# Kernel optimization log

Hardware: AMD Instinct MI355X
Metric: run time of the kernel (lower is better)

Reference implementation:

```python
import jax, jax.numpy as jnp
import numpy as np

N_NODES = 100000
D_FEAT = 256
INPUT_ATT = 256


def setup_inputs() -> dict:
    key = jax.random.key(0)
    k1, k2, k3, kw, kh = jax.random.split(key, 5)
    x1 = jax.random.normal(k1, (N_NODES, D_FEAT), dtype=jnp.float32)
    x2 = jax.random.normal(k2, (N_NODES, D_FEAT), dtype=jnp.float32)
    x3 = jax.random.normal(k3, (N_NODES, D_FEAT), dtype=jnp.float32)
    # xavier-normal-like init for parameters
    W = jax.random.normal(kw, (INPUT_ATT, N_NODES), dtype=jnp.float32) * float(np.sqrt(2.0 / (INPUT_ATT + N_NODES)))
    h_n = jax.random.normal(kh, (1, INPUT_ATT), dtype=jnp.float32) * float(np.sqrt(2.0 / (1 + INPUT_ATT)))
    return {"x1": x1, "x2": x2, "x3": x3, "W": W, "h_n": h_n}


def reference(x1, x2, x3, W, h_n):
    # temp_k = tanh(W @ x_k): (input_att, D) for each of the 3 views
    t1 = jnp.tanh(W @ x1)
    t2 = jnp.tanh(W @ x2)
    t3 = jnp.tanh(W @ x3)
    # per-view, per-feature score: (1, D) each -> stacked (3, D)
    scores = jnp.concatenate([h_n @ t1, h_n @ t2, h_n @ t3], axis=0)  # (3, D)
    beta = jax.nn.softmax(scores, axis=0)  # softmax over the 3 views, per feature column
    # fused broadcast weighted sum (replaces the per-row Python loop)
    out = beta[0] * x1 + beta[1] * x2 + beta[2] * x3  # (N, D)
    return out
```

## Files before the change

### kernel.cpp

```cpp
#include <hip/hip_runtime.h>
#include <hip/hip_bf16.h>

#define N_NODES 100000
#define D_FEAT  256
#define N_ATT   256

typedef __bf16 bf16x4 __attribute__((ext_vector_type(4)));
typedef __bf16 bf16x8 __attribute__((ext_vector_type(8)));
typedef float  f32x16 __attribute__((ext_vector_type(16)));

__device__ __forceinline__ unsigned short bf16_rne(float f) {
    unsigned u = __float_as_uint(f);
    return (unsigned short)((u + 0x7fffu + ((u >> 16) & 1u)) >> 16);
}

__device__ __forceinline__ void split1(float f, unsigned short& h, unsigned short& l) {
    h = bf16_rne(f);
    float fh = __uint_as_float((unsigned)h << 16);
    l = (unsigned short)(__float_as_uint(f - fh) >> 16);
}

__device__ __forceinline__ bf16x8 ld8(const unsigned short* p) {
    bf16x4 lo = *(const bf16x4*)p;
    bf16x4 hi = *(const bf16x4*)(p + 4);
    return __builtin_shufflevector(lo, hi, 0, 1, 2, 3, 4, 5, 6, 7);
}

#define LDK 36

__global__ __launch_bounds__(512, 4) void gemm_split(
    const float* __restrict__ x1, const float* __restrict__ x2,
    const float* __restrict__ x3, const float* __restrict__ W,
    float* __restrict__ C, int chunk)
{
    extern __shared__ unsigned short lds[];
    unsigned short* Ah = lds;
    unsigned short* Al = Ah + 128 * LDK;
    unsigned short* Bh = Al + 128 * LDK;

    const int bid = blockIdx.x;
    const int s   = bid / 6;
    const int pos = bid % 6;
    const int v   = pos >> 1;
    const int m0  = (pos & 1) * 128;
    const float* __restrict__ X = (v == 0) ? x1 : (v == 1) ? x2 : x3;

    const int ks = s * chunk;
    const int ke = min(ks + chunk, N_NODES);

    const int tid  = threadIdx.x;
    const int lane = tid & 63;
    const int wave = tid >> 6;
    const int mstrip = (wave & 3) * 32;
    const int nhalf  = (wave >> 2) * 128;

    const int a_m  = tid >> 3;
    const int a_kk = (tid & 7) * 4;
    const int b_n64 = tid & 63;
    const int b_nb  = (tid >> 8) * 64;
    const int b_kq  = ((tid >> 6) & 3) ^ ((tid >> 3) & 3);

    const int l31 = lane & 31;
    const int khalf = (lane >> 5) * 8;

    f32x16 acc[4] = {};

    float4 pa[2];
    float  pb[4][4];

    auto issue = [&](int kg0) {
        #pragma unroll
        for (int p = 0; p < 2; ++p) {
            int kg = kg0 + a_kk;
            pa[p] = make_float4(0.f, 0.f, 0.f, 0.f);
            if (kg < ke)
                pa[p] = *(const float4*)(W + (size_t)(m0 + p * 64 + a_m) * N_NODES + kg);
        }
        #pragma unroll
        for (int p = 0; p < 4; ++p) {
            int n  = (p >> 1) * 128 + b_nb + b_n64;
            int kg = kg0 + (p & 1) * 16 + b_kq * 4;
            pb[p][0] = pb[p][1] = pb[p][2] = pb[p][3] = 0.f;
            if (kg < ke) {
                const float* xp = X + (size_t)kg * D_FEAT + n;
                pb[p][0] = xp[0];
                pb[p][1] = xp[D_FEAT];
                pb[p][2] = xp[2 * D_FEAT];
                pb[p][3] = xp[3 * D_FEAT];
            }
        }
    };

    issue(ks);

    for (int k0 = ks; k0 < ke; k0 += 32) {
        __syncthreads();

        #pragma unroll
        for (int p = 0; p < 2; ++p) {
            ushort4 h4, l4;
            split1(pa[p].x, h4.x, l4.x); split1(pa[p].y, h4.y, l4.y);
            split1(pa[p].z, h4.z, l4.z); split1(pa[p].w, h4.w, l4.w);
            int m = p * 64 + a_m;
            *(ushort4*)(Ah + m * LDK + a_kk) = h4;
            *(ushort4*)(Al + m * LDK + a_kk) = l4;
        }
        #pragma unroll
        for (int p = 0; p < 4; ++p) {
            int n  = (p >> 1) * 128 + b_nb + b_n64;
            int kb = (p & 1) * 16 + b_kq * 4;
            ushort4 h4;
            h4.x = bf16_rne(pb[p][0]); h4.y = bf16_rne(pb[p][1]);
            h4.z = bf16_rne(pb[p][2]); h4.w = bf16_rne(pb[p][3]);
            *(ushort4*)(Bh + n * LDK + kb) = h4;
        }

        if (k0 + 32 < ke) issue(k0 + 32);

        __syncthreads();

        #pragma unroll
        for (int kk = 0; kk < 2; ++kk) {
            int kf = kk * 16 + khalf;
            int arow = mstrip + l31;
            bf16x8 ah = ld8(Ah + arow * LDK + kf);
            bf16x8 al = ld8(Al + arow * LDK + kf);
            #pragma unroll
            for (int nb = 0; nb < 4; ++nb) {
                int brow = nhalf + nb * 32 + l31;
                bf16x8 bh = ld8(Bh + brow * LDK + kf);
                acc[nb] = __builtin_amdgcn_mfma_f32_32x32x16_bf16(ah, bh, acc[nb], 0, 0, 0);
                acc[nb] = __builtin_amdgcn_mfma_f32_32x32x16_bf16(al, bh, acc[nb], 0, 0, 0);
            }
        }
    }

    float* Cv = C + v * (N_ATT * D_FEAT);
    const int col = l31;
    const int rbase = 4 * (lane >> 5);
    #pragma unroll
    for (int nb = 0; nb < 4; ++nb) {
        int gj = nhalf + nb * 32 + col;
        #pragma unroll
        for (int r = 0; r < 16; ++r) {
            int row = (r & 3) + 8 * (r >> 2) + rbase;
            int gi = m0 + mstrip + row;
            unsafeAtomicAdd(Cv + gi * D_FEAT + gj, acc[nb][r]);
        }
    }
}

__global__ __launch_bounds__(256) void score_kernel(
    const float* __restrict__ C, const float* __restrict__ h,
    float* __restrict__ scores)
{
    const int v  = blockIdx.x >> 3;
    const int ig = blockIdx.x & 7;
    const int j  = threadIdx.x;
    const float* Cv = C + v * (N_ATT * D_FEAT);
    float s = 0.f;
    #pragma unroll 4
    for (int i = ig * 32; i < ig * 32 + 32; ++i)
        s += h[i] * tanhf(Cv[i * D_FEAT + j]);
    unsafeAtomicAdd(scores + v * D_FEAT + j, s);
}

__device__ __forceinline__ float blend(float xa, float xb, float xc,
                                       float t0, float t1, float t2) {
    float m = fmaxf(t0, fmaxf(t1, t2));
    float e0 = __expf(t0 - m), e1 = __expf(t1 - m), e2 = __expf(t2 - m);
    float inv = 1.0f / (e0 + e1 + e2);
    return (e0 * xa + e1 * xb + e2 * xc) * inv;
}

__global__ __launch_bounds__(256) void out_kernel(
    const float* __restrict__ x1, const float* __restrict__ x2,
    const float* __restrict__ x3, const float* __restrict__ scores,
    float* __restrict__ out)
{
    size_t idx  = (size_t)blockIdx.x * 256 + threadIdx.x;
    size_t base = idx * 4;
    int j = (int)(base & (D_FEAT - 1));
    float4 a = *(const float4*)(x1 + base);
    float4 b = *(const float4*)(x2 + base);
    float4 c = *(const float4*)(x3 + base);
    float4 s0 = *(const float4*)(scores + j);
    float4 s1 = *(const float4*)(scores + D_FEAT + j);
    float4 s2 = *(const float4*)(scores + 2 * D_FEAT + j);
    float4 o;
    o.x = blend(a.x, b.x, c.x, s0.x, s1.x, s2.x);
    o.y = blend(a.y, b.y, c.y, s0.y, s1.y, s2.y);
    o.z = blend(a.z, b.z, c.z, s0.z, s1.z, s2.z);
    o.w = blend(a.w, b.w, c.w, s0.w, s1.w, s2.w);
    *(float4*)(out + base) = o;
}

extern "C" void kernel_launch(void* const* d_in, const int* in_sizes, int n_in,
                              void* d_out, int out_size, void* d_ws, size_t ws_size,
                              hipStream_t stream) {
    const float* x1 = (const float*)d_in[0];
    const float* x2 = (const float*)d_in[1];
    const float* x3 = (const float*)d_in[2];
    const float* W  = (const float*)d_in[3];
    const float* h  = (const float*)d_in[4];
    float* out = (float*)d_out;

    float* C      = (float*)d_ws;
    float* scores = C + 3 * N_ATT * D_FEAT;

    hipMemsetAsync(d_ws, 0, (3 * N_ATT * D_FEAT + 3 * D_FEAT) * sizeof(float), stream);

    const int chunk = 1180;
    gemm_split<<<dim3(510), dim3(512), 512 * LDK * 2, stream>>>(x1, x2, x3, W, C, chunk);

    score_kernel<<<dim3(24), dim3(256), 0, stream>>>(C, h, scores);

    out_kernel<<<dim3((N_NODES * D_FEAT) / (4 * 256)), dim3(256), 0, stream>>>(
        x1, x2, x3, scores, out);
}
```

Before: 505.5 us.

## Double-buffer LDS tiles in split-K GEMM with one barrier per step

Splits the GEMM k-loop into stage and compute steps over two LDS buffers. Each iteration now issues the next global loads, runs MFMAs on the current buffer, then converts and stores into the other buffer, so it needs one barrier per step instead of two. The chunk size becomes a multiple of 32, which lets the per-element bounds checks on W and X loads be dropped. The cost is double the LDS per block, which may lower how many blocks fit on a CU, and the code now relies on N being divisible by the tile size.

```diff
diff --git a/kernel.cpp b/kernel.cpp
--- a/kernel.cpp
+++ b/kernel.cpp
@@ -27,6 +27,7 @@
 }
 
 #define LDK 36
+#define BUF_SHORTS (512 * LDK)
 
 __global__ __launch_bounds__(512, 4) void gemm_split(
     const float* __restrict__ x1, const float* __restrict__ x2,
@@ -34,9 +35,6 @@
     float* __restrict__ C, int chunk)
 {
     extern __shared__ unsigned short lds[];
-    unsigned short* Ah = lds;
-    unsigned short* Al = Ah + 128 * LDK;
-    unsigned short* Bh = Al + 128 * LDK;
 
     const int bid = blockIdx.x;
     const int s   = bid / 6;
@@ -54,48 +52,41 @@
     const int mstrip = (wave & 3) * 32;
     const int nhalf  = (wave >> 2) * 128;
 
-    const int a_m  = tid >> 3;
-    const int a_kk = (tid & 7) * 4;
+    const int a_m   = tid >> 3;
+    const int a_kk  = (tid & 7) * 4;
     const int b_n64 = tid & 63;
     const int b_nb  = (tid >> 8) * 64;
-    const int b_kq  = ((tid >> 6) & 3) ^ ((tid >> 3) & 3);
+    const int b_kq4 = (((tid >> 6) & 3) ^ ((tid >> 3) & 3)) * 4;
 
     const int l31 = lane & 31;
     const int khalf = (lane >> 5) * 8;
 
     f32x16 acc[4] = {};
-
     float4 pa[2];
     float  pb[4][4];
 
+    const float* Wb = W + (size_t)(m0 + a_m) * N_NODES + a_kk;
+
     auto issue = [&](int kg0) {
         #pragma unroll
-        for (int p = 0; p < 2; ++p) {
-            int kg = kg0 + a_kk;
-            pa[p] = make_float4(0.f, 0.f, 0.f, 0.f);
-            if (kg < ke)
-                pa[p] = *(const float4*)(W + (size_t)(m0 + p * 64 + a_m) * N_NODES + kg);
-        }
+        for (int p = 0; p < 2; ++p)
+            pa[p] = *(const float4*)(Wb + (size_t)p * 64 * N_NODES + kg0);
         #pragma unroll
         for (int p = 0; p < 4; ++p) {
             int n  = (p >> 1) * 128 + b_nb + b_n64;
-            int kg = kg0 + (p & 1) * 16 + b_kq * 4;
-            pb[p][0] = pb[p][1] = pb[p][2] = pb[p][3] = 0.f;
-            if (kg < ke) {
-                const float* xp = X + (size_t)kg * D_FEAT + n;
-                pb[p][0] = xp[0];
-                pb[p][1] = xp[D_FEAT];
-                pb[p][2] = xp[2 * D_FEAT];
-                pb[p][3] = xp[3 * D_FEAT];
-            }
+            int kg = kg0 + (p & 1) * 16 + b_kq4;
+            const float* xp = X + (size_t)kg * D_FEAT + n;
+            pb[p][0] = xp[0];
+            pb[p][1] = xp[D_FEAT];
+            pb[p][2] = xp[2 * D_FEAT];
+            pb[p][3] = xp[3 * D_FEAT];
         }
     };
 
-    issue(ks);
-
-    for (int k0 = ks; k0 < ke; k0 += 32) {
-        __syncthreads();
-
+    auto stage = [&](unsigned short* buf) {
+        unsigned short* Ah = buf;
+        unsigned short* Al = buf + 128 * LDK;
+        unsigned short* Bh = buf + 256 * LDK;
         #pragma unroll
         for (int p = 0; p < 2; ++p) {
             ushort4 h4, l4;
@@ -108,17 +99,18 @@
         #pragma unroll
         for (int p = 0; p < 4; ++p) {
             int n  = (p >> 1) * 128 + b_nb + b_n64;
-            int kb = (p & 1) * 16 + b_kq * 4;
+            int kb = (p & 1) * 16 + b_kq4;
             ushort4 h4;
             h4.x = bf16_rne(pb[p][0]); h4.y = bf16_rne(pb[p][1]);
             h4.z = bf16_rne(pb[p][2]); h4.w = bf16_rne(pb[p][3]);
             *(ushort4*)(Bh + n * LDK + kb) = h4;
         }
-
-        if (k0 + 32 < ke) issue(k0 + 32);
-
-        __syncthreads();
-
+    };
+
+    auto compute = [&](const unsigned short* buf) {
+        const unsigned short* Ah = buf;
+        const unsigned short* Al = buf + 128 * LDK;
+        const unsigned short* Bh = buf + 256 * LDK;
         #pragma unroll
         for (int kk = 0; kk < 2; ++kk) {
             int kf = kk * 16 + khalf;
@@ -133,6 +125,23 @@
                 acc[nb] = __builtin_amdgcn_mfma_f32_32x32x16_bf16(al, bh, acc[nb], 0, 0, 0);
             }
         }
+    };
+
+    issue(ks);
+    stage(lds);
+    __syncthreads();
+
+    int q = 0;
+    for (int k0 = ks;;) {
+        int k1 = k0 + 32;
+        bool more = (k1 < ke);
+        if (more) issue(k1);
+        compute(lds + q * BUF_SHORTS);
+        if (!more) break;
+        stage(lds + (q ^ 1) * BUF_SHORTS);
+        __syncthreads();
+        q ^= 1;
+        k0 = k1;
     }
 
     float* Cv = C + v * (N_ATT * D_FEAT);
@@ -210,8 +219,8 @@
 
     hipMemsetAsync(d_ws, 0, (3 * N_ATT * D_FEAT + 3 * D_FEAT) * sizeof(float), stream);
 
-    const int chunk = 1180;
-    gemm_split<<<dim3(510), dim3(512), 512 * LDK * 2, stream>>>(x1, x2, x3, W, C, chunk);
+    const int chunk = 1184;
+    gemm_split<<<dim3(510), dim3(512), 2 * BUF_SHORTS * 2, stream>>>(x1, x2, x3, W, C, chunk);
 
     score_kernel<<<dim3(24), dim3(256), 0, stream>>>(C, h, scores);
 
```

Result: no change. 500.4 us (-1.0%).
